# Kernel optimization log

Measured on AMD Instinct MI355X. Metric: run time of the kernel, lower is better.

## Reference

```python
import jax, jax.numpy as jnp
import numpy as np

W0_SIREN = 30.0  # omega_0 used in sine activations

HID = [64, 64, 256, 256, 256]
IN_DIM = 65   # 64 feat channels + 1 time channel
OUT_DIM = 64


def _siren_params(key):
    dims = [IN_DIM] + HID + [OUT_DIM]
    params = []
    for i in range(len(dims) - 1):
        fan_in, fan_out = dims[i], dims[i + 1]
        key, kw, kb = jax.random.split(key, 3)
        if i == 0:
            bound = 1.0 / fan_in
        else:
            bound = np.sqrt(6.0 / fan_in) / W0_SIREN
        W = jax.random.uniform(kw, (fan_out, fan_in), jnp.float32, -bound, bound)
        b = jax.random.uniform(kb, (fan_out,), jnp.float32, -bound, bound)
        params.append((W, b))
    return params


def setup_inputs() -> dict:
    key = jax.random.key(0)
    k_feat, k_t, k_p = jax.random.split(key, 3)
    feat = jax.random.normal(k_feat, (2, 64, 192, 320), jnp.float32)
    times = jax.random.uniform(k_t, (3,), jnp.float32)
    params = _siren_params(k_p)
    inp = {"feat": feat, "times": times}
    for i, (W, b) in enumerate(params):
        inp[f"w{i}"] = W
        inp[f"b{i}"] = b
    return inp


def _gather_full_grid(feat):
    """Nearest grid_sample (align_corners=False) at pixel-center coords over the full grid.
    Returns [B, H*W, C]."""
    B, C, H, W = feat.shape
    # make_coord pixel centers in [-1, 1]
    ys = -1.0 + (2.0 * jnp.arange(H, dtype=jnp.float32) + 1.0) / H
    xs = -1.0 + (2.0 * jnp.arange(W, dtype=jnp.float32) + 1.0) / W
    gy, gx = jnp.meshgrid(ys, xs, indexing="ij")          # [H, W] each
    gy, gx = gy.reshape(-1), gx.reshape(-1)               # [qs]
    # grid_sample nearest, align_corners=False unnormalization
    iy = jnp.clip(jnp.round(((gy + 1.0) * H - 1.0) / 2.0).astype(jnp.int32), 0, H - 1)
    ix = jnp.clip(jnp.round(((gx + 1.0) * W - 1.0) / 2.0).astype(jnp.int32), 0, W - 1)
    q = feat[:, :, iy, ix]                                # [B, C, qs] gather
    return jnp.transpose(q, (0, 2, 1))                    # [B, qs, C]


def _siren_mlp(x, ws, bs):
    h = x
    n = len(ws)
    for i in range(n - 1):
        h = jnp.sin(W0_SIREN * (h @ ws[i].T + bs[i]))
    return h @ ws[n - 1].T + bs[n - 1]                    # outermost linear


def reference(feat, times, w0, b0, w1, b1, w2, b2, w3, b3, w4, b4, w5, b5):
    ws = [w0, w1, w2, w3, w4, w5]
    bs = [b0, b1, b2, b3, b4, b5]
    B, C, H, W = feat.shape
    qs = H * W
    q_feat = _gather_full_grid(feat)                      # [B, qs, 64]
    preds = []
    for c in range(3):  # Training==True branch: 3 time stamps
        t = times[c]
        pe = jnp.full((B, qs, 1), 1.0, feat.dtype) * t    # time channel
        enc = jnp.concatenate([q_feat, pe], axis=-1)      # [B, qs, 65]
        out = _siren_mlp(enc.reshape(B * qs, IN_DIM), ws, bs)  # [B*qs, 64]
        # F.fold with kernel_size=1 == reshape back to spatial map
        pred = out.reshape(B, qs, OUT_DIM).transpose(0, 2, 1).reshape(B, OUT_DIM, H, W)
        preds.append(pred)
    return jnp.stack(preds, axis=0)                       # [3, B, 64, H, W]
```

## Files before the change

kernel.cpp:

```cpp
#include <hip/hip_runtime.h>

typedef __bf16 bf16_t;
typedef bf16_t bf16x8 __attribute__((ext_vector_type(8)));
typedef float f32x4 __attribute__((ext_vector_type(4)));
typedef unsigned short u16;
typedef unsigned int u32;

static constexpr int kHW = 192 * 320;
static constexpr int kS  = 264;

__device__ __forceinline__ u16 f2bf(float f) {
  u32 u = __float_as_uint(f);
  return (u16)((u + 0x7FFFu + ((u >> 16) & 1u)) >> 16);
}

static constexpr int OFF_W0 = 0;
static constexpr int OFF_W1 = 4096;
static constexpr int OFF_W2 = 8192;
static constexpr int OFF_W3 = 24576;
static constexpr int OFF_W4 = 90112;
static constexpr int OFF_W5 = 155648;
static constexpr int W_TOTAL = 172032;

__global__ void convert_weights(const float* __restrict__ w0, const float* __restrict__ w1,
                                const float* __restrict__ w2, const float* __restrict__ w3,
                                const float* __restrict__ w4, const float* __restrict__ w5,
                                u16* __restrict__ wb) {
  int i = blockIdx.x * 256 + threadIdx.x;
  float v;
  if (i < OFF_W1)      { int o = i >> 6, k = i & 63; v = w0[o * 65 + k]; }
  else if (i < OFF_W2) { v = w1[i - OFF_W1]; }
  else if (i < OFF_W3) { v = w2[i - OFF_W2]; }
  else if (i < OFF_W4) { v = w3[i - OFF_W3]; }
  else if (i < OFF_W5) { v = w4[i - OFF_W4]; }
  else                 { v = w5[i - OFF_W5]; }
  wb[i] = f2bf(v);
}

template<int K, int N, bool LAST>
__device__ __forceinline__ void layer_fn(const u16* __restrict__ wb,
                                         const float* bias_lds,
                                         const u16* act_in, u16* act_out,
                                         float* __restrict__ out_base) {
  constexpr int KT = K / 32;
  constexpr int OT = N / 64;
  const int tid  = threadIdx.x;
  const int lane = tid & 63;
  const int wave = tid >> 6;
  const int l15  = lane & 15;
  const int quad = lane >> 4;

  bf16x8 wf[OT][KT];
#pragma unroll
  for (int ot = 0; ot < OT; ++ot) {
    const int o = (wave * OT + ot) * 16 + l15;
#pragma unroll
    for (int ks = 0; ks < KT; ++ks)
      wf[ot][ks] = *reinterpret_cast<const bf16x8*>(wb + o * K + ks * 32 + quad * 8);
  }
  f32x4 bv[OT];
#pragma unroll
  for (int ot = 0; ot < OT; ++ot)
    bv[ot] = *reinterpret_cast<const f32x4*>(bias_lds + (wave * OT + ot) * 16 + quad * 4);

#pragma unroll
  for (int pt = 0; pt < 4; ++pt) {
    bf16x8 af[KT];
#pragma unroll
    for (int ks = 0; ks < KT; ++ks)
      af[ks] = *reinterpret_cast<const bf16x8*>(act_in + (pt * 16 + l15) * kS + ks * 32 + quad * 8);

    f32x4 acc[OT];
#pragma unroll
    for (int ot = 0; ot < OT; ++ot) acc[ot] = bv[ot];
#pragma unroll
    for (int ks = 0; ks < KT; ++ks)
#pragma unroll
      for (int ot = 0; ot < OT; ++ot)
        acc[ot] = __builtin_amdgcn_mfma_f32_16x16x32_bf16(wf[ot][ks], af[ks], acc[ot], 0, 0, 0);

    const int p = pt * 16 + l15;
#pragma unroll
    for (int ot = 0; ot < OT; ++ot) {
      if constexpr (LAST) {
        const int o = (wave * OT + ot) * 16 + quad * 4;
        float* dst = out_base + (size_t)o * kHW + p;
#pragma unroll
        for (int r = 0; r < 4; ++r) dst[(size_t)r * kHW] = acc[ot][r];
      } else {
        u16 h0 = f2bf(__sinf(30.0f * acc[ot][0]));
        u16 h1 = f2bf(__sinf(30.0f * acc[ot][1]));
        u16 h2 = f2bf(__sinf(30.0f * acc[ot][2]));
        u16 h3 = f2bf(__sinf(30.0f * acc[ot][3]));
        uint2 v;
        v.x = (u32)h0 | ((u32)h1 << 16);
        v.y = (u32)h2 | ((u32)h3 << 16);
        *reinterpret_cast<uint2*>(act_out + p * kS + (wave * OT + ot) * 16 + quad * 4) = v;
      }
    }
  }
}

__global__ void __launch_bounds__(256, 2)
siren_main(const float* __restrict__ feat, const float* __restrict__ times,
           const float* __restrict__ w0f,
           const float* __restrict__ b0, const float* __restrict__ b1,
           const float* __restrict__ b2, const float* __restrict__ b3,
           const float* __restrict__ b4, const float* __restrict__ b5,
           const u16* __restrict__ wb, float* __restrict__ out) {
  __shared__ __align__(16) u16 actA[64 * kS];
  __shared__ __align__(16) u16 actB[64 * kS];
  __shared__ __align__(16) float bias_lds[960];

  const int tid = threadIdx.x;
  const int bid = blockIdx.x;
  const int c   = bid / 1920;
  const int pb  = bid % 1920;
  const int p0  = pb * 64;
  const int bq  = p0 / kHW;
  const int hw0 = p0 % kHW;

  const float t = times[c];

  if (tid < 64) {
    bias_lds[tid]       = b0[tid] + t * w0f[tid * 65 + 64];
    bias_lds[64 + tid]  = b1[tid];
    bias_lds[896 + tid] = b5[tid];
  }
  bias_lds[128 + tid] = b2[tid];
  bias_lds[384 + tid] = b3[tid];
  bias_lds[640 + tid] = b4[tid];

  {
    const float* fbase = feat + (size_t)bq * 64 * kHW + hw0;
#pragma unroll
    for (int it = 0; it < 16; ++it) {
      int ch = it * 4 + (tid >> 6);
      int p  = tid & 63;
      actA[p * kS + ch] = f2bf(fbase[(size_t)ch * kHW + p]);
    }
  }
  __syncthreads();

  float* out_base = out + (size_t)(c * 2 + bq) * 64 * kHW + hw0;

  layer_fn<64, 64, false>(wb + OFF_W0, bias_lds + 0, actA, actB, nullptr);
  __syncthreads();
  layer_fn<64, 64, false>(wb + OFF_W1, bias_lds + 64, actB, actA, nullptr);
  __syncthreads();
  layer_fn<64, 256, false>(wb + OFF_W2, bias_lds + 128, actA, actB, nullptr);
  __syncthreads();
  layer_fn<256, 256, false>(wb + OFF_W3, bias_lds + 384, actB, actA, nullptr);
  __syncthreads();
  layer_fn<256, 256, false>(wb + OFF_W4, bias_lds + 640, actA, actB, nullptr);
  __syncthreads();
  layer_fn<256, 64, true>(wb + OFF_W5, bias_lds + 896, actB, actA, out_base);
}

extern "C" void kernel_launch(void* const* d_in, const int* in_sizes, int n_in,
                              void* d_out, int out_size, void* d_ws, size_t ws_size,
                              hipStream_t stream) {
  const float* feat  = (const float*)d_in[0];
  const float* times = (const float*)d_in[1];
  const float* w0 = (const float*)d_in[2];
  const float* b0 = (const float*)d_in[3];
  const float* w1 = (const float*)d_in[4];
  const float* b1 = (const float*)d_in[5];
  const float* w2 = (const float*)d_in[6];
  const float* b2 = (const float*)d_in[7];
  const float* w3 = (const float*)d_in[8];
  const float* b3 = (const float*)d_in[9];
  const float* w4 = (const float*)d_in[10];
  const float* b4 = (const float*)d_in[11];
  const float* w5 = (const float*)d_in[12];
  const float* b5 = (const float*)d_in[13];
  u16* wb = (u16*)d_ws;
  float* out = (float*)d_out;

  convert_weights<<<W_TOTAL / 256, 256, 0, stream>>>(w0, w1, w2, w3, w4, w5, wb);
  siren_main<<<5760, 256, 0, stream>>>(feat, times, w0, b0, b1, b2, b3, b4, b5, wb, out);
}
```

Measured before the change: 407.3 us.

## Restructure SIREN kernel with 8 waves, swizzled LDS, prescaled weights and fract-sin

After: 403.1 us. About the same (-1.0%).

```diff
diff --git a/kernel.cpp b/kernel.cpp
--- a/kernel.cpp
+++ b/kernel.cpp
@@ -1,4 +1,5 @@
 #include <hip/hip_runtime.h>
+#include <hip/hip_bf16.h>
 
 typedef __bf16 bf16_t;
 typedef bf16_t bf16x8 __attribute__((ext_vector_type(8)));
@@ -7,11 +8,18 @@
 typedef unsigned int u32;
 
 static constexpr int kHW = 192 * 320;
-static constexpr int kS  = 264;
+static constexpr float kC = 4.77464829275686f;
 
 __device__ __forceinline__ u16 f2bf(float f) {
   u32 u = __float_as_uint(f);
   return (u16)((u + 0x7FFFu + ((u >> 16) & 1u)) >> 16);
+}
+
+__device__ __forceinline__ u32 pack2(float a, float b) {
+  __hip_bfloat162 h = __float22bfloat162_rn(make_float2(a, b));
+  union { __hip_bfloat162 h2; u32 u; } cv;
+  cv.h2 = h;
+  return cv.u;
 }
 
 static constexpr int OFF_W0 = 0;
@@ -21,95 +29,101 @@
 static constexpr int OFF_W4 = 90112;
 static constexpr int OFF_W5 = 155648;
 static constexpr int W_TOTAL = 172032;
+static constexpr int B_TOTAL = 1024;
 
 __global__ void convert_weights(const float* __restrict__ w0, const float* __restrict__ w1,
                                 const float* __restrict__ w2, const float* __restrict__ w3,
                                 const float* __restrict__ w4, const float* __restrict__ w5,
-                                u16* __restrict__ wb) {
+                                const float* __restrict__ b0, const float* __restrict__ b1,
+                                const float* __restrict__ b2, const float* __restrict__ b3,
+                                const float* __restrict__ b4, const float* __restrict__ b5,
+                                u16* __restrict__ wb, float* __restrict__ bws) {
   int i = blockIdx.x * 256 + threadIdx.x;
-  float v;
-  if (i < OFF_W1)      { int o = i >> 6, k = i & 63; v = w0[o * 65 + k]; }
-  else if (i < OFF_W2) { v = w1[i - OFF_W1]; }
-  else if (i < OFF_W3) { v = w2[i - OFF_W2]; }
-  else if (i < OFF_W4) { v = w3[i - OFF_W3]; }
-  else if (i < OFF_W5) { v = w4[i - OFF_W4]; }
-  else                 { v = w5[i - OFF_W5]; }
-  wb[i] = f2bf(v);
-}
-
-template<int K, int N, bool LAST>
-__device__ __forceinline__ void layer_fn(const u16* __restrict__ wb,
-                                         const float* bias_lds,
+  if (i < W_TOTAL) {
+    float v, s = kC;
+    if (i < OFF_W1)      { int o = i >> 6, k = i & 63; v = w0[o * 65 + k]; }
+    else if (i < OFF_W2) { v = w1[i - OFF_W1]; }
+    else if (i < OFF_W3) { v = w2[i - OFF_W2]; }
+    else if (i < OFF_W4) { v = w3[i - OFF_W3]; }
+    else if (i < OFF_W5) { v = w4[i - OFF_W4]; }
+    else                 { v = w5[i - OFF_W5]; s = 1.0f; }
+    wb[i] = f2bf(v * s);
+  } else {
+    int j = i - W_TOTAL;
+    float v;
+    if (j < 64)       v = kC * b0[j];
+    else if (j < 128) v = kC * w0[(j - 64) * 65 + 64];
+    else if (j < 192) v = kC * b1[j - 128];
+    else if (j < 448) v = kC * b2[j - 192];
+    else if (j < 704) v = kC * b3[j - 448];
+    else if (j < 960) v = kC * b4[j - 704];
+    else              v = b5[j - 960];
+    bws[j] = v;
+  }
+}
+
+template<int K, int NOT, int NPT, bool LAST>
+__device__ __forceinline__ void layer_fn(const u16* __restrict__ wb, const float* bias,
                                          const u16* act_in, u16* act_out,
-                                         float* __restrict__ out_base) {
+                                         float* __restrict__ out_base,
+                                         int o_tile0, int pt0, int lane) {
   constexpr int KT = K / 32;
-  constexpr int OT = N / 64;
-  const int tid  = threadIdx.x;
-  const int lane = tid & 63;
-  const int wave = tid >> 6;
   const int l15  = lane & 15;
   const int quad = lane >> 4;
-
-  bf16x8 wf[OT][KT];
-#pragma unroll
-  for (int ot = 0; ot < OT; ++ot) {
-    const int o = (wave * OT + ot) * 16 + l15;
+  const int sw   = l15 & 7;
+
+  bf16x8 wf[NOT][KT];
+  f32x4  bv[NOT];
+#pragma unroll
+  for (int ot = 0; ot < NOT; ++ot) {
+    const int o = (o_tile0 + ot) * 16 + l15;
 #pragma unroll
     for (int ks = 0; ks < KT; ++ks)
       wf[ot][ks] = *reinterpret_cast<const bf16x8*>(wb + o * K + ks * 32 + quad * 8);
-  }
-  f32x4 bv[OT];
-#pragma unroll
-  for (int ot = 0; ot < OT; ++ot)
-    bv[ot] = *reinterpret_cast<const f32x4*>(bias_lds + (wave * OT + ot) * 16 + quad * 4);
-
-#pragma unroll
-  for (int pt = 0; pt < 4; ++pt) {
+    bv[ot] = *reinterpret_cast<const f32x4*>(bias + (o_tile0 + ot) * 16 + quad * 4);
+  }
+
+#pragma unroll 1
+  for (int ip = 0; ip < NPT; ++ip) {
+    const int p = (pt0 + ip) * 16 + l15;
     bf16x8 af[KT];
 #pragma unroll
     for (int ks = 0; ks < KT; ++ks)
-      af[ks] = *reinterpret_cast<const bf16x8*>(act_in + (pt * 16 + l15) * kS + ks * 32 + quad * 8);
-
-    f32x4 acc[OT];
-#pragma unroll
-    for (int ot = 0; ot < OT; ++ot) acc[ot] = bv[ot];
-#pragma unroll
-    for (int ks = 0; ks < KT; ++ks)
-#pragma unroll
-      for (int ot = 0; ot < OT; ++ot)
-        acc[ot] = __builtin_amdgcn_mfma_f32_16x16x32_bf16(wf[ot][ks], af[ks], acc[ot], 0, 0, 0);
-
-    const int p = pt * 16 + l15;
-#pragma unroll
-    for (int ot = 0; ot < OT; ++ot) {
+      af[ks] = *reinterpret_cast<const bf16x8*>(act_in + p * 256 + (((ks * 4 + quad) ^ sw) * 8));
+
+#pragma unroll
+    for (int ot = 0; ot < NOT; ++ot) {
+      f32x4 acc = bv[ot];
+#pragma unroll
+      for (int ks = 0; ks < KT; ++ks)
+        acc = __builtin_amdgcn_mfma_f32_16x16x32_bf16(wf[ot][ks], af[ks], acc, 0, 0, 0);
+
       if constexpr (LAST) {
-        const int o = (wave * OT + ot) * 16 + quad * 4;
+        const int o = (o_tile0 + ot) * 16 + quad * 4;
         float* dst = out_base + (size_t)o * kHW + p;
 #pragma unroll
-        for (int r = 0; r < 4; ++r) dst[(size_t)r * kHW] = acc[ot][r];
+        for (int r = 0; r < 4; ++r) dst[(size_t)r * kHW] = acc[r];
       } else {
-        u16 h0 = f2bf(__sinf(30.0f * acc[ot][0]));
-        u16 h1 = f2bf(__sinf(30.0f * acc[ot][1]));
-        u16 h2 = f2bf(__sinf(30.0f * acc[ot][2]));
-        u16 h3 = f2bf(__sinf(30.0f * acc[ot][3]));
+        float s0 = __builtin_amdgcn_sinf(__builtin_amdgcn_fractf(acc[0]));
+        float s1 = __builtin_amdgcn_sinf(__builtin_amdgcn_fractf(acc[1]));
+        float s2 = __builtin_amdgcn_sinf(__builtin_amdgcn_fractf(acc[2]));
+        float s3 = __builtin_amdgcn_sinf(__builtin_amdgcn_fractf(acc[3]));
         uint2 v;
-        v.x = (u32)h0 | ((u32)h1 << 16);
-        v.y = (u32)h2 | ((u32)h3 << 16);
-        *reinterpret_cast<uint2*>(act_out + p * kS + (wave * OT + ot) * 16 + quad * 4) = v;
+        v.x = pack2(s0, s1);
+        v.y = pack2(s2, s3);
+        const int g = (o_tile0 + ot) * 2 + (quad >> 1);
+        *reinterpret_cast<uint2*>(act_out + p * 256 + ((g ^ sw) * 8) + (quad & 1) * 4) = v;
       }
     }
   }
 }
 
-__global__ void __launch_bounds__(256, 2)
+__global__ void __launch_bounds__(512, 4)
 siren_main(const float* __restrict__ feat, const float* __restrict__ times,
-           const float* __restrict__ w0f,
-           const float* __restrict__ b0, const float* __restrict__ b1,
-           const float* __restrict__ b2, const float* __restrict__ b3,
-           const float* __restrict__ b4, const float* __restrict__ b5,
-           const u16* __restrict__ wb, float* __restrict__ out) {
-  __shared__ __align__(16) u16 actA[64 * kS];
-  __shared__ __align__(16) u16 actB[64 * kS];
+           const u16* __restrict__ wb, const float* __restrict__ bws,
+           float* __restrict__ out) {
+  __shared__ __align__(16) u16 actA[64 * 256];
+  __shared__ __align__(16) u16 actB[64 * 256];
   __shared__ __align__(16) float bias_lds[960];
 
   const int tid = threadIdx.x;
@@ -119,42 +133,46 @@
   const int p0  = pb * 64;
   const int bq  = p0 / kHW;
   const int hw0 = p0 % kHW;
-
   const float t = times[c];
 
-  if (tid < 64) {
-    bias_lds[tid]       = b0[tid] + t * w0f[tid * 65 + 64];
-    bias_lds[64 + tid]  = b1[tid];
-    bias_lds[896 + tid] = b5[tid];
-  }
-  bias_lds[128 + tid] = b2[tid];
-  bias_lds[384 + tid] = b3[tid];
-  bias_lds[640 + tid] = b4[tid];
+  if (tid < 64) bias_lds[tid] = bws[tid] + t * bws[64 + tid];
+  for (int i = tid; i < 896; i += 512) bias_lds[64 + i] = bws[128 + i];
 
   {
     const float* fbase = feat + (size_t)bq * 64 * kHW + hw0;
-#pragma unroll
-    for (int it = 0; it < 16; ++it) {
-      int ch = it * 4 + (tid >> 6);
-      int p  = tid & 63;
-      actA[p * kS + ch] = f2bf(fbase[(size_t)ch * kHW + p]);
-    }
-  }
-  __syncthreads();
-
+    const int p = tid & 63;
+    const int g = tid >> 6;
+    float v[8];
+#pragma unroll
+    for (int j = 0; j < 8; ++j) v[j] = fbase[(size_t)(g * 8 + j) * kHW + p];
+    uint4 pk;
+    pk.x = pack2(v[0], v[1]);
+    pk.y = pack2(v[2], v[3]);
+    pk.z = pack2(v[4], v[5]);
+    pk.w = pack2(v[6], v[7]);
+    *reinterpret_cast<uint4*>(actA + p * 256 + ((g ^ (p & 7)) * 8)) = pk;
+  }
+  __syncthreads();
+
+  const int wave = tid >> 6;
+  const int lane = tid & 63;
   float* out_base = out + (size_t)(c * 2 + bq) * 64 * kHW + hw0;
 
-  layer_fn<64, 64, false>(wb + OFF_W0, bias_lds + 0, actA, actB, nullptr);
-  __syncthreads();
-  layer_fn<64, 64, false>(wb + OFF_W1, bias_lds + 64, actB, actA, nullptr);
-  __syncthreads();
-  layer_fn<64, 256, false>(wb + OFF_W2, bias_lds + 128, actA, actB, nullptr);
-  __syncthreads();
-  layer_fn<256, 256, false>(wb + OFF_W3, bias_lds + 384, actB, actA, nullptr);
-  __syncthreads();
-  layer_fn<256, 256, false>(wb + OFF_W4, bias_lds + 640, actA, actB, nullptr);
-  __syncthreads();
-  layer_fn<256, 64, true>(wb + OFF_W5, bias_lds + 896, actB, actA, out_base);
+  const int ot64  = wave & 3;
+  const int pt64  = (wave >> 2) * 2;
+  const int ot256 = wave * 2;
+
+  layer_fn<64, 1, 2, false>(wb + OFF_W0, bias_lds + 0,   actA, actB, nullptr, ot64, pt64, lane);
+  __syncthreads();
+  layer_fn<64, 1, 2, false>(wb + OFF_W1, bias_lds + 64,  actB, actA, nullptr, ot64, pt64, lane);
+  __syncthreads();
+  layer_fn<64, 2, 4, false>(wb + OFF_W2, bias_lds + 128, actA, actB, nullptr, ot256, 0, lane);
+  __syncthreads();
+  layer_fn<256, 2, 4, false>(wb + OFF_W3, bias_lds + 384, actB, actA, nullptr, ot256, 0, lane);
+  __syncthreads();
+  layer_fn<256, 2, 4, false>(wb + OFF_W4, bias_lds + 640, actA, actB, nullptr, ot256, 0, lane);
+  __syncthreads();
+  layer_fn<256, 1, 2, true >(wb + OFF_W5, bias_lds + 896, actB, nullptr, out_base, ot64, pt64, lane);
 }
 
 extern "C" void kernel_launch(void* const* d_in, const int* in_sizes, int n_in,
@@ -174,9 +192,11 @@
   const float* b4 = (const float*)d_in[11];
   const float* w5 = (const float*)d_in[12];
   const float* b5 = (const float*)d_in[13];
-  u16* wb = (u16*)d_ws;
+  u16*   wb  = (u16*)d_ws;
+  float* bws = (float*)((char*)d_ws + (size_t)W_TOTAL * 2);
   float* out = (float*)d_out;
 
-  convert_weights<<<W_TOTAL / 256, 256, 0, stream>>>(w0, w1, w2, w3, w4, w5, wb);
-  siren_main<<<5760, 256, 0, stream>>>(feat, times, w0, b0, b1, b2, b3, b4, b5, wb, out);
-}
+  convert_weights<<<(W_TOTAL + B_TOTAL) / 256, 256, 0, stream>>>(
+      w0, w1, w2, w3, w4, w5, b0, b1, b2, b3, b4, b5, wb, bws);
+  siren_main<<<5760, 512, 0, stream>>>(feat, times, wb, bws, out);
+}
```
